# Kernel optimization log

Measured on AMD Instinct MI355X. Metric: run time of the kernel, lower is better.

## Reference

```python
import jax, jax.numpy as jnp
import numpy as np

B, T, D_IN, H = 128, 256, 512, 1024

def setup_inputs() -> dict:
    key = jax.random.key(0)
    ks = jax.random.split(key, 12)
    s = 1.0 / np.sqrt(H)
    return {
        "input": jax.random.normal(ks[0], (B, T, D_IN), jnp.float32),
        "h0": jax.random.normal(ks[1], (B, H), jnp.float32),
        "c0": jax.random.normal(ks[2], (B, H), jnp.float32),
        "ctx": jax.random.normal(ks[3], (B, T, H), jnp.float32),
        "srcmask": jax.random.randint(ks[4], (B, T), 0, 2).astype(bool),
        "W_ih": jax.random.uniform(ks[5], (4 * H, D_IN), jnp.float32, -s, s),
        "W_hh": jax.random.uniform(ks[6], (4 * H, H), jnp.float32, -s, s),
        "b_ih": jax.random.uniform(ks[7], (4 * H,), jnp.float32, -s, s),
        "b_hh": jax.random.uniform(ks[8], (4 * H,), jnp.float32, -s, s),
        "W_attn": jax.random.uniform(ks[9], (H, H), jnp.float32, -s, s),
        "W_out": jax.random.uniform(ks[10], (H, 2 * H), jnp.float32, -s, s),
    }


def reference(input, h0, c0, ctx, srcmask, W_ih, W_hh, b_ih, b_hh, W_attn, W_out):
    def step(carry, x_t):
        h, c = carry
        # LSTMCell: gate order i, f, g, o (PyTorch convention)
        gates = x_t @ W_ih.T + b_ih + h @ W_hh.T + b_hh  # [B, 4H]
        i_g, f_g, g_g, o_g = jnp.split(gates, 4, axis=-1)
        cy = jax.nn.sigmoid(f_g) * c + jax.nn.sigmoid(i_g) * jnp.tanh(g_g)
        hy = jax.nn.sigmoid(o_g) * jnp.tanh(cy)
        # Bilinear attention: score(K_j, q) = K_j^T (W_attn q)
        q = hy @ W_attn.T                                   # [B, H]
        scores = jnp.einsum("blh,bh->bl", ctx, q)          # [B, L]
        scores = jnp.where(srcmask, -jnp.inf, scores)
        probs = jax.nn.softmax(scores, axis=-1)
        wctx = jnp.einsum("bl,blh->bh", probs, ctx)        # [B, H]
        h_tilde = jnp.tanh(jnp.concatenate([wctx, hy], axis=-1) @ W_out.T)
        return (h_tilde, cy), h_tilde

    xs = jnp.transpose(input, (1, 0, 2))  # [T, B, D_IN]
    (h_f, c_f), outs = jax.lax.scan(step, (h0, c0), xs)
    output = jnp.transpose(outs, (1, 0, 2))  # [B, T, H]
    return (output, h_f, c_f)
```

## Files before the change

### kernel.cpp

```cpp
#include <hip/hip_runtime.h>
#include <hip/hip_bf16.h>
#include <math.h>

#define B_  128
#define T_  256
#define DIN 512
#define H_  1024

typedef __attribute__((ext_vector_type(8))) short bf16x8;
typedef __attribute__((ext_vector_type(4))) float f32x4;

#define GLD_LDS16(gsrc, ldst) \
  __builtin_amdgcn_global_load_lds((const __attribute__((address_space(1))) void*)(gsrc), \
                                   (__attribute__((address_space(3))) void*)(ldst), 16, 0, 0)

__device__ __forceinline__ void split_bf16(float v, __hip_bfloat16* hi, __hip_bfloat16* lo) {
    __hip_bfloat16 h = __float2bfloat16(v);
    *hi = h;
    *lo = __float2bfloat16(v - __bfloat162float(h));
}

template<int N> __device__ __forceinline__ void waitvm() {
    if constexpr (N == 0)       asm volatile("s_waitcnt vmcnt(0)" ::: "memory");
    else if constexpr (N == 10) asm volatile("s_waitcnt vmcnt(10)" ::: "memory");
    else static_assert(N == 0 || N == 10, "add vmcnt literal");
}

__global__ void bias_sum_k(const float* __restrict__ a, const float* __restrict__ b,
                           float* __restrict__ o, int n) {
    int i = blockIdx.x * blockDim.x + threadIdx.x;
    if (i < n) o[i] = a[i] + b[i];
}

__global__ void detect_mask_k(const int* __restrict__ m, int nwords, int* __restrict__ flag) {
    __shared__ int bad;
    if (threadIdx.x == 0) bad = 0;
    __syncthreads();
    for (int i = threadIdx.x; i < nwords; i += blockDim.x) {
        unsigned v = (unsigned)m[i];
        if (v > 1u) bad = 1;
    }
    __syncthreads();
    if (threadIdx.x == 0) flag[0] = bad ? 0 : 1;
}

__global__ void cvt_split_k(const float* __restrict__ s, __hip_bfloat16* __restrict__ hi,
                            __hip_bfloat16* __restrict__ lo, int n) {
    int i = blockIdx.x * 256 + threadIdx.x;
    if (i < n) split_bf16(s[i], hi + i, lo + i);
}

__global__ void wg_split_k(const float* __restrict__ Wih, const float* __restrict__ Whh,
                           __hip_bfloat16* __restrict__ Wh, __hip_bfloat16* __restrict__ Wl) {
    int i = blockIdx.x * 256 + threadIdx.x;
    int n = i / 1536, c = i - n * 1536;
    float v = (c < DIN) ? Wih[n * DIN + c] : Whh[n * H_ + (c - DIN)];
    split_bf16(v, Wh + i, Wl + i);
}

__device__ __forceinline__ void cvtx_body(int i, const float* __restrict__ xsrc,
                                          __hip_bfloat16* __restrict__ xh,
                                          __hip_bfloat16* __restrict__ xl) {
    int b = i >> 9, c = i & 511;
    split_bf16(xsrc[(size_t)b * (T_ * DIN) + c], xh + i, xl + i);
}

__global__ void cvtx_k(const float* __restrict__ xsrc, __hip_bfloat16* __restrict__ xh,
                       __hip_bfloat16* __restrict__ xl) {
    cvtx_body(blockIdx.x * 256 + threadIdx.x, xsrc, xh, xl);
}

template<int NT>
__global__ __launch_bounds__(256)
void mfma_gemm_k(const __hip_bfloat16* __restrict__ A1h, const __hip_bfloat16* __restrict__ A1l,
                 long lda1, int K1,
                 const __hip_bfloat16* __restrict__ A2h, const __hip_bfloat16* __restrict__ A2l,
                 long lda2,
                 const __hip_bfloat16* __restrict__ Wh, const __hip_bfloat16* __restrict__ Wl,
                 long ldw,
                 float* __restrict__ Cpart, long ldc, long pstride)
{
    constexpr int APL = 128 * 64 * 2;
    constexpr int BPL = 32 * 64 * 2;
    constexpr int BUFB = 2 * APL + 2 * BPL;
    __shared__ __attribute__((aligned(16))) char lds[3 * BUFB];

    const int tid = threadIdx.x;
    const int l = tid & 63, w = tid >> 6;
    const int n0 = blockIdx.x * 32;
    const int kbase = blockIdx.y * (NT * 64);
    const int wm = (w >> 1) * 64, wn = (w & 1) * 16;

    auto stage = [&](int buf, int kt) {
        char* base = lds + buf * BUFB;
        const int kb = kbase + kt * 64;
        #pragma unroll
        for (int p = 0; p < 2; ++p) {
            const __hip_bfloat16* A1 = p ? A1l : A1h;
            const __hip_bfloat16* A2 = p ? A2l : A2h;
            #pragma unroll
            for (int j = 0; j < 4; ++j) {
                int c = j * 256 + tid;
                int row = c >> 3, slot = c & 7;
                int e = kb + ((slot ^ (row & 7)) << 3);
                const __hip_bfloat16* src = (e < K1) ? (A1 + (long)row * lda1 + e)
                                                     : (A2 + (long)row * lda2 + (e - K1));
                GLD_LDS16(src, base + p * APL + ((j * 256 + (tid & 192)) << 4));
            }
            {
                int row = tid >> 3, slot = tid & 7;
                int e = kb + ((slot ^ (row & 7)) << 3);
                const __hip_bfloat16* src = (p ? Wl : Wh) + (long)(n0 + row) * ldw + e;
                GLD_LDS16(src, base + 2 * APL + p * BPL + ((tid & 192) << 4));
            }
        }
    };

    f32x4 acc[4] = {};

    stage(0, 0);
    if (NT > 1) stage(1, 1);

    for (int kt = 0; kt < NT; ++kt) {
        if (kt + 1 < NT) waitvm<10>(); else waitvm<0>();
        __builtin_amdgcn_s_barrier();
        __builtin_amdgcn_sched_barrier(0);
        if (kt + 2 < NT) stage((kt + 2) % 3, kt + 2);

        const char* base = lds + (kt % 3) * BUFB;
        #pragma unroll
        for (int ks = 0; ks < 2; ++ks) {
            bf16x8 afh[4], afl[4], bh, bl;
            #pragma unroll
            for (int mi = 0; mi < 4; ++mi) {
                int row = wm + mi * 16 + (l & 15);
                int slot = (l >> 4) + ks * 4;
                int off = row * 128 + ((slot ^ (row & 7)) << 4);
                afh[mi] = *(const bf16x8*)(base + off);
                afl[mi] = *(const bf16x8*)(base + APL + off);
            }
            {
                int row = wn + (l & 15);
                int slot = (l >> 4) + ks * 4;
                int off = row * 128 + ((slot ^ (row & 7)) << 4);
                bh = *(const bf16x8*)(base + 2 * APL + off);
                bl = *(const bf16x8*)(base + 2 * APL + BPL + off);
            }
            #pragma unroll
            for (int mi = 0; mi < 4; ++mi) {
                acc[mi] = __builtin_amdgcn_mfma_f32_16x16x32_bf16(afh[mi], bh, acc[mi], 0, 0, 0);
                acc[mi] = __builtin_amdgcn_mfma_f32_16x16x32_bf16(afl[mi], bh, acc[mi], 0, 0, 0);
                acc[mi] = __builtin_amdgcn_mfma_f32_16x16x32_bf16(afh[mi], bl, acc[mi], 0, 0, 0);
            }
        }
    }

    float* Cb = Cpart + (long)blockIdx.y * pstride;
    const int n = n0 + wn + (l & 15);
    #pragma unroll
    for (int mi = 0; mi < 4; ++mi) {
        int mbase = wm + mi * 16 + (l >> 4) * 4;
        #pragma unroll
        for (int r = 0; r < 4; ++r)
            Cb[(long)(mbase + r) * ldc + n] = acc[mi][r];
    }
}

__device__ __forceinline__ float sigmoidf_(float x) { return 1.f / (1.f + expf(-x)); }

__global__ __launch_bounds__(256)
void cell_cvtx_k(const float* __restrict__ gpart,
                 const float* __restrict__ bsum,
                 const float* __restrict__ cprev, float* __restrict__ cy,
                 __hip_bfloat16* __restrict__ AoBh, __hip_bfloat16* __restrict__ AoBl,
                 float* __restrict__ cf,
                 const float* __restrict__ xnext,
                 __hip_bfloat16* __restrict__ xh, __hip_bfloat16* __restrict__ xl)
{
    int bid = blockIdx.x;
    if (bid < 512) {
        int idx = bid * 256 + threadIdx.x;
        int b = idx >> 10, j = idx & 1023;
        const float* g0 = gpart + ((size_t)b << 12);
        const float* g1 = g0 + (size_t)128 * 4096;
        float ig = sigmoidf_(g0[j]        + g1[j]        + bsum[j]);
        float fg = sigmoidf_(g0[1024 + j] + g1[1024 + j] + bsum[1024 + j]);
        float gg = tanhf    (g0[2048 + j] + g1[2048 + j] + bsum[2048 + j]);
        float og = sigmoidf_(g0[3072 + j] + g1[3072 + j] + bsum[3072 + j]);
        float c = fg * cprev[idx] + ig * gg;
        float h = og * tanhf(c);
        cy[idx] = c;
        split_bf16(h, AoBh + (size_t)b * 2048 + 1024 + j, AoBl + (size_t)b * 2048 + 1024 + j);
        if (cf) cf[idx] = c;
    } else if (xnext) {
        cvtx_body((bid - 512) * 256 + threadIdx.x, xnext, xh, xl);
    }
}

__global__ __launch_bounds__(256)
void attn_k(const float* __restrict__ ctx, const float* __restrict__ qpart,
            const void* __restrict__ maskp, const int* __restrict__ mflag,
            __hip_bfloat16* __restrict__ AoBh, __hip_bfloat16* __restrict__ AoBl)
{
    constexpr int L = T_, H = H_;
    int b = blockIdx.x;
    const float* cb = ctx + (size_t)b * L * H;
    int tid = threadIdx.x, l = tid & 63, w = tid >> 6;
    int mode = mflag[0];

    float rq[16];
    #pragma unroll
    for (int j = 0; j < 16; ++j) {
        size_t o = (size_t)b * H + l + j * 64;
        rq[j] = qpart[o] + qpart[o + 131072] + qpart[o + 262144] + qpart[o + 393216];
    }

    float m = -INFINITY, s = 0.f, acc[16] = {};
    for (int li = w; li < L; li += 4) {
        bool msk = mode ? (((const int*)maskp)[b * L + li] != 0)
                        : (((const unsigned char*)maskp)[b * L + li] != 0);
        if (msk) continue;
        const float* cr = cb + (size_t)li * H;
        float rc[16], d = 0.f;
        #pragma unroll
        for (int j = 0; j < 16; ++j) { rc[j] = cr[l + j * 64]; d += rc[j] * rq[j]; }
        #pragma unroll
        for (int off = 1; off < 64; off <<= 1) d += __shfl_xor(d, off);
        float mn = fmaxf(m, d);
        float f = expf(m - mn);
        float p = expf(d - mn);
        s = s * f + p;
        #pragma unroll
        for (int j = 0; j < 16; ++j) acc[j] = acc[j] * f + p * rc[j];
        m = mn;
    }

    __shared__ float sacc[4][H_];
    __shared__ float sms[4][2];
    #pragma unroll
    for (int j = 0; j < 16; ++j) sacc[w][l + j * 64] = acc[j];
    if (l == 0) { sms[w][0] = m; sms[w][1] = s; }
    __syncthreads();

    float M = fmaxf(fmaxf(sms[0][0], sms[1][0]), fmaxf(sms[2][0], sms[3][0]));
    float fw[4], S = 0.f;
    #pragma unroll
    for (int ww = 0; ww < 4; ++ww) { fw[ww] = expf(sms[ww][0] - M); S += fw[ww] * sms[ww][1]; }
    float inv = 1.f / S;
    for (int k = tid; k < H; k += 256) {
        float a = sacc[0][k] * fw[0] + sacc[1][k] * fw[1] + sacc[2][k] * fw[2] + sacc[3][k] * fw[3];
        split_bf16(a * inv, AoBh + (size_t)b * 2048 + k, AoBl + (size_t)b * 2048 + k);
    }
}

__global__ __launch_bounds__(256)
void outred_k(const float* __restrict__ opart,
              __hip_bfloat16* __restrict__ hth, __hip_bfloat16* __restrict__ htl,
              float* __restrict__ outp,
              float* __restrict__ hf)
{
    int idx = blockIdx.x * 256 + threadIdx.x;
    int b = idx >> 10, j = idx & 1023;
    float v = opart[idx] + opart[idx + 131072] + opart[idx + 262144] + opart[idx + 393216];
    v = tanhf(v);
    split_bf16(v, hth + idx, htl + idx);
    outp[(size_t)b * (T_ * H_) + j] = v;
    if (hf) hf[idx] = v;
}

extern "C" void kernel_launch(void* const* d_in, const int* in_sizes, int n_in,
                              void* d_out, int out_size, void* d_ws, size_t ws_size,
                              hipStream_t stream)
{
    const float* input  = (const float*)d_in[0];
    const float* h0     = (const float*)d_in[1];
    const float* c0     = (const float*)d_in[2];
    const float* ctx    = (const float*)d_in[3];
    const void*  srcmask= d_in[4];
    const float* W_ih   = (const float*)d_in[5];
    const float* W_hh   = (const float*)d_in[6];
    const float* b_ih   = (const float*)d_in[7];
    const float* b_hh   = (const float*)d_in[8];
    const float* W_attn = (const float*)d_in[9];
    const float* W_out  = (const float*)d_in[10];

    constexpr int B = B_, T = T_, D = DIN, H = H_;

    float* f = (float*)d_ws;
    float* bsum  = f; f += 4 * H;
    float* cbuf  = f; f += (size_t)B * H;
    float* gpart = f; f += (size_t)2 * B * 4 * H;
    float* qpart = f; f += (size_t)4 * B * H;
    float* opart = f; f += (size_t)4 * B * H;
    int*   mflag = (int*)f; f += 64;
    __hip_bfloat16* p = (__hip_bfloat16*)f;
    __hip_bfloat16* Wgh = p; p += (size_t)4 * H * (D + H);
    __hip_bfloat16* Wgl = p; p += (size_t)4 * H * (D + H);
    __hip_bfloat16* Wah = p; p += (size_t)H * H;
    __hip_bfloat16* Wal = p; p += (size_t)H * H;
    __hip_bfloat16* Woh = p; p += (size_t)H * 2 * H;
    __hip_bfloat16* Wol = p; p += (size_t)H * 2 * H;
    __hip_bfloat16* hth = p; p += (size_t)B * H;
    __hip_bfloat16* htl = p; p += (size_t)B * H;
    __hip_bfloat16* AoBh = p; p += (size_t)B * 2 * H;
    __hip_bfloat16* AoBl = p; p += (size_t)B * 2 * H;
    __hip_bfloat16* xth[2], *xtl[2];
    xth[0] = p; p += (size_t)B * D;
    xtl[0] = p; p += (size_t)B * D;
    xth[1] = p; p += (size_t)B * D;
    xtl[1] = p; p += (size_t)B * D;

    float* out = (float*)d_out;
    float* hf  = out + (size_t)B * T * H;
    float* cf  = hf + (size_t)B * H;

    hipMemcpyAsync(cbuf, c0, (size_t)B * H * sizeof(float), hipMemcpyDeviceToDevice, stream);
    bias_sum_k<<<dim3(16), dim3(256), 0, stream>>>(b_ih, b_hh, bsum, 4 * H);
    detect_mask_k<<<dim3(1), dim3(256), 0, stream>>>((const int*)srcmask, B * T / 4, mflag);
    wg_split_k<<<dim3(4 * H * (D + H) / 256), dim3(256), 0, stream>>>(W_ih, W_hh, Wgh, Wgl);
    cvt_split_k<<<dim3(H * H / 256), dim3(256), 0, stream>>>(W_attn, Wah, Wal, H * H);
    cvt_split_k<<<dim3(H * 2 * H / 256), dim3(256), 0, stream>>>(W_out, Woh, Wol, H * 2 * H);
    cvt_split_k<<<dim3(B * H / 256), dim3(256), 0, stream>>>(h0, hth, htl, B * H);
    cvtx_k<<<dim3(B * D / 256), dim3(256), 0, stream>>>(input, xth[0], xtl[0]);

    dim3 blk(256);
    for (int t = 0; t < T; ++t) {
        int sl = t & 1, sn = sl ^ 1;

        mfma_gemm_k<12><<<dim3(128, 2), blk, 0, stream>>>(
            xth[sl], xtl[sl], D, D,
            hth, htl, H,
            Wgh, Wgl, D + H,
            gpart, 4 * H, (long)B * 4 * H);

        cell_cvtx_k<<<dim3(768), blk, 0, stream>>>(
            gpart, bsum, cbuf, cbuf, AoBh, AoBl, (t == T - 1) ? cf : nullptr,
            (t + 1 < T) ? input + (size_t)(t + 1) * D : nullptr, xth[sn], xtl[sn]);

        mfma_gemm_k<4><<<dim3(32, 4), blk, 0, stream>>>(
            AoBh + H, AoBl + H, 2 * H, 2 * H,
            AoBh + H, AoBl + H, 2 * H,
            Wah, Wal, H,
            qpart, H, (long)B * H);

        attn_k<<<dim3(B), blk, 0, stream>>>(ctx, qpart, srcmask, mflag, AoBh, AoBl);

        mfma_gemm_k<8><<<dim3(32, 4), blk, 0, stream>>>(
            AoBh, AoBl, 2 * H, 2 * H,
            AoBh, AoBl, 2 * H,
            Woh, Wol, 2 * H,
            opart, H, (long)B * H);

        outred_k<<<dim3(512), blk, 0, stream>>>(
            opart, hth, htl, out + (size_t)t * H, (t == T - 1) ? hf : nullptr);
    }
}
```

Baseline: 18.29 ms.

## Fuse LSTM cell into gate GEMM epilogue and output tanh into out GEMM

After: 21.53 ms. 17.7% more time.

```diff
diff --git a/kernel.cpp b/kernel.cpp
--- a/kernel.cpp
+++ b/kernel.cpp
@@ -14,22 +14,22 @@
   __builtin_amdgcn_global_load_lds((const __attribute__((address_space(1))) void*)(gsrc), \
                                    (__attribute__((address_space(3))) void*)(ldst), 16, 0, 0)
 
+#define WAITVM_(n) asm volatile("s_waitcnt vmcnt(" #n ")" ::: "memory")
+#define WAITVM(n) WAITVM_(n)
+
 __device__ __forceinline__ void split_bf16(float v, __hip_bfloat16* hi, __hip_bfloat16* lo) {
     __hip_bfloat16 h = __float2bfloat16(v);
     *hi = h;
     *lo = __float2bfloat16(v - __bfloat162float(h));
 }
 
-template<int N> __device__ __forceinline__ void waitvm() {
-    if constexpr (N == 0)       asm volatile("s_waitcnt vmcnt(0)" ::: "memory");
-    else if constexpr (N == 10) asm volatile("s_waitcnt vmcnt(10)" ::: "memory");
-    else static_assert(N == 0 || N == 10, "add vmcnt literal");
-}
-
-__global__ void bias_sum_k(const float* __restrict__ a, const float* __restrict__ b,
-                           float* __restrict__ o, int n) {
-    int i = blockIdx.x * blockDim.x + threadIdx.x;
-    if (i < n) o[i] = a[i] + b[i];
+__device__ __forceinline__ float sigmoidf_(float x) { return 1.f / (1.f + expf(-x)); }
+
+__global__ void bsum_perm_k(const float* __restrict__ bi, const float* __restrict__ bh,
+                            float* __restrict__ o) {
+    int c = blockIdx.x * 256 + threadIdx.x;
+    int srow = ((c & 3) << 10) | (c >> 2);
+    o[c] = bi[srow] + bh[srow];
 }
 
 __global__ void detect_mask_k(const int* __restrict__ m, int nwords, int* __restrict__ flag) {
@@ -50,150 +50,174 @@
     if (i < n) split_bf16(s[i], hi + i, lo + i);
 }
 
-__global__ void wg_split_k(const float* __restrict__ Wih, const float* __restrict__ Whh,
-                           __hip_bfloat16* __restrict__ Wh, __hip_bfloat16* __restrict__ Wl) {
-    int i = blockIdx.x * 256 + threadIdx.x;
-    int n = i / 1536, c = i - n * 1536;
-    float v = (c < DIN) ? Wih[n * DIN + c] : Whh[n * H_ + (c - DIN)];
+__global__ void wgp_split_k(const float* __restrict__ Wih, const float* __restrict__ Whh,
+                            __hip_bfloat16* __restrict__ Wh, __hip_bfloat16* __restrict__ Wl) {
+    long i = (long)blockIdx.x * 256 + threadIdx.x;
+    int c = (int)(i / 1536), k = (int)(i - (long)c * 1536);
+    int srow = ((c & 3) << 10) | (c >> 2);
+    float v = (k < DIN) ? Wih[(long)srow * DIN + k] : Whh[(long)srow * H_ + (k - DIN)];
     split_bf16(v, Wh + i, Wl + i);
-}
-
-__device__ __forceinline__ void cvtx_body(int i, const float* __restrict__ xsrc,
-                                          __hip_bfloat16* __restrict__ xh,
-                                          __hip_bfloat16* __restrict__ xl) {
-    int b = i >> 9, c = i & 511;
-    split_bf16(xsrc[(size_t)b * (T_ * DIN) + c], xh + i, xl + i);
 }
 
 __global__ void cvtx_k(const float* __restrict__ xsrc, __hip_bfloat16* __restrict__ xh,
                        __hip_bfloat16* __restrict__ xl) {
-    cvtx_body(blockIdx.x * 256 + threadIdx.x, xsrc, xh, xl);
-}
-
-template<int NT>
+    int i = blockIdx.x * 256 + threadIdx.x;
+    int b = i >> 9, c = i & 511;
+    split_bf16(xsrc[(long)b * (T_ * DIN) + c], xh + i, xl + i);
+}
+
+constexpr int APL = 128 * 64 * 2;
+constexpr int BPL = 32 * 64 * 2;
+constexpr int BUFB = 2 * APL + 2 * BPL;
+constexpr int LDSZ = 3 * BUFB;
+
+#define GEMM_CORE(NT, NW2, BNV, VMID, NB, KSP, A1H, A1L, LDA1, K1V, A2H, A2L, LDA2, WHP, WLP, LDW) \
+    const int n0_ = (NB) * (BNV); \
+    const int kbase_ = (KSP) * ((NT) * 64); \
+    const int wm_ = (NW2) ? (w >> 1) * 64 : w * 32; \
+    const int wn_ = (NW2) ? (w & 1) * 16 : 0; \
+    auto stage = [&](int buf, int kt) { \
+        char* base = lds + buf * BUFB; \
+        const int kb = kbase_ + kt * 64; \
+        _Pragma("unroll") \
+        for (int pp = 0; pp < 2; ++pp) { \
+            const __hip_bfloat16* A1 = pp ? (A1L) : (A1H); \
+            const __hip_bfloat16* A2 = pp ? (A2L) : (A2H); \
+            _Pragma("unroll") \
+            for (int j = 0; j < 4; ++j) { \
+                int c = j * 256 + tid; \
+                int row = c >> 3, sl2 = c & 7; \
+                int e = kb + ((sl2 ^ (row & 7)) << 3); \
+                const __hip_bfloat16* src = (e < (K1V)) ? (A1 + (long)row * (LDA1) + e) \
+                                                        : (A2 + (long)row * (LDA2) + (e - (K1V))); \
+                GLD_LDS16(src, base + pp * APL + ((j * 256 + (tid & 192)) << 4)); \
+            } \
+            if (tid < (BNV) * 8) { \
+                int row = tid >> 3, sl2 = tid & 7; \
+                int e = kb + ((sl2 ^ (row & 7)) << 3); \
+                const __hip_bfloat16* src = (pp ? (WLP) : (WHP)) + (long)(n0_ + row) * (LDW) + e; \
+                GLD_LDS16(src, base + 2 * APL + pp * BPL + ((tid & 192) << 4)); \
+            } \
+        } \
+    }; \
+    f32x4 acc[4] = {}; \
+    stage(0, 0); \
+    if ((NT) > 1) stage(1, 1); \
+    for (int kt = 0; kt < (NT); ++kt) { \
+        if (kt + 1 < (NT)) { WAITVM(VMID); } else { WAITVM(0); } \
+        __builtin_amdgcn_s_barrier(); \
+        __builtin_amdgcn_sched_barrier(0); \
+        if (kt + 2 < (NT)) stage((kt + 2) % 3, kt + 2); \
+        const char* base = lds + (kt % 3) * BUFB; \
+        _Pragma("unroll") \
+        for (int ks = 0; ks < 2; ++ks) { \
+            bf16x8 afh[4], afl[4], bh, bl; \
+            _Pragma("unroll") \
+            for (int mi = 0; mi < ((NW2) ? 4 : 2); ++mi) { \
+                int row = wm_ + mi * 16 + (l & 15); \
+                int sl2 = (l >> 4) + ks * 4; \
+                int off = row * 128 + ((sl2 ^ (row & 7)) << 4); \
+                afh[mi] = *(const bf16x8*)(base + off); \
+                afl[mi] = *(const bf16x8*)(base + APL + off); \
+            } \
+            { \
+                int row = wn_ + (l & 15); \
+                int sl2 = (l >> 4) + ks * 4; \
+                int off = row * 128 + ((sl2 ^ (row & 7)) << 4); \
+                bh = *(const bf16x8*)(base + 2 * APL + off); \
+                bl = *(const bf16x8*)(base + 2 * APL + BPL + off); \
+            } \
+            _Pragma("unroll") \
+            for (int mi = 0; mi < ((NW2) ? 4 : 2); ++mi) { \
+                acc[mi] = __builtin_amdgcn_mfma_f32_16x16x32_bf16(afh[mi], bh, acc[mi], 0, 0, 0); \
+                acc[mi] = __builtin_amdgcn_mfma_f32_16x16x32_bf16(afl[mi], bh, acc[mi], 0, 0, 0); \
+                acc[mi] = __builtin_amdgcn_mfma_f32_16x16x32_bf16(afh[mi], bl, acc[mi], 0, 0, 0); \
+            } \
+        } \
+    }
+
 __global__ __launch_bounds__(256)
-void mfma_gemm_k(const __hip_bfloat16* __restrict__ A1h, const __hip_bfloat16* __restrict__ A1l,
-                 long lda1, int K1,
-                 const __hip_bfloat16* __restrict__ A2h, const __hip_bfloat16* __restrict__ A2l,
-                 long lda2,
-                 const __hip_bfloat16* __restrict__ Wh, const __hip_bfloat16* __restrict__ Wl,
-                 long ldw,
-                 float* __restrict__ Cpart, long ldc, long pstride)
-{
-    constexpr int APL = 128 * 64 * 2;
-    constexpr int BPL = 32 * 64 * 2;
-    constexpr int BUFB = 2 * APL + 2 * BPL;
-    __shared__ __attribute__((aligned(16))) char lds[3 * BUFB];
-
+void gemm_g_k(const __hip_bfloat16* __restrict__ xh, const __hip_bfloat16* __restrict__ xl,
+              const __hip_bfloat16* __restrict__ hh, const __hip_bfloat16* __restrict__ hl,
+              const __hip_bfloat16* __restrict__ Wgh, const __hip_bfloat16* __restrict__ Wgl,
+              const float* __restrict__ bsump, float* __restrict__ cbuf,
+              __hip_bfloat16* __restrict__ AoBh, __hip_bfloat16* __restrict__ AoBl,
+              float* __restrict__ cf,
+              const float* __restrict__ input, int t,
+              __hip_bfloat16* __restrict__ nxh, __hip_bfloat16* __restrict__ nxl)
+{
+    __shared__ __attribute__((aligned(16))) char lds[LDSZ];
+    const int blk = blockIdx.x, tid = threadIdx.x;
+    const int l = tid & 63, w = tid >> 6;
+
+    GEMM_CORE(24, 1, 32, 10, blk, 0,
+              xh, xl, DIN, DIN, hh, hl, H_, Wgh, Wgl, (DIN + H_));
+
+    __syncthreads();
+    float* sg = (float*)lds;
+    {
+        float bv = bsump[n0_ + wn_ + (l & 15)];
+        #pragma unroll
+        for (int mi = 0; mi < 4; ++mi) {
+            int rbase = wm_ + mi * 16 + (l >> 4) * 4;
+            int col = wn_ + (l & 15);
+            #pragma unroll
+            for (int r = 0; r < 4; ++r)
+                sg[(rbase + r) * 36 + col] = acc[mi][r] + bv;
+        }
+    }
+    __syncthreads();
+
+    #pragma unroll
+    for (int k = 0; k < 4; ++k) {
+        int ci = k * 256 + tid;
+        int b = ci >> 3, jp = ci & 7;
+        float4 g4 = *(const float4*)&sg[b * 36 + jp * 4];
+        int j = blk * 8 + jp;
+        long idx = (long)b * H_ + j;
+        float ig = sigmoidf_(g4.x);
+        float fg = sigmoidf_(g4.y);
+        float gg = tanhf(g4.z);
+        float og = sigmoidf_(g4.w);
+        float c = fg * cbuf[idx] + ig * gg;
+        float h = og * tanhf(c);
+        cbuf[idx] = c;
+        split_bf16(h, AoBh + (long)b * 2048 + 1024 + j, AoBl + (long)b * 2048 + 1024 + j);
+        if (cf) cf[idx] = c;
+    }
+
+    if (t + 1 < T_) {
+        #pragma unroll
+        for (int k = 0; k < 2; ++k) {
+            int i2 = blk * 512 + k * 256 + tid;
+            int b2 = i2 >> 9, col = i2 & 511;
+            float v = input[((long)b2 * T_ + (t + 1)) * DIN + col];
+            split_bf16(v, nxh + i2, nxl + i2);
+        }
+    }
+}
+
+__global__ __launch_bounds__(256)
+void gemm_q_k(const __hip_bfloat16* __restrict__ AoBh, const __hip_bfloat16* __restrict__ AoBl,
+              const __hip_bfloat16* __restrict__ Wah, const __hip_bfloat16* __restrict__ Wal,
+              float* __restrict__ qpart)
+{
+    __shared__ __attribute__((aligned(16))) char lds[LDSZ];
     const int tid = threadIdx.x;
     const int l = tid & 63, w = tid >> 6;
-    const int n0 = blockIdx.x * 32;
-    const int kbase = blockIdx.y * (NT * 64);
-    const int wm = (w >> 1) * 64, wn = (w & 1) * 16;
-
-    auto stage = [&](int buf, int kt) {
-        char* base = lds + buf * BUFB;
-        const int kb = kbase + kt * 64;
-        #pragma unroll
-        for (int p = 0; p < 2; ++p) {
-            const __hip_bfloat16* A1 = p ? A1l : A1h;
-            const __hip_bfloat16* A2 = p ? A2l : A2h;
-            #pragma unroll
-            for (int j = 0; j < 4; ++j) {
-                int c = j * 256 + tid;
-                int row = c >> 3, slot = c & 7;
-                int e = kb + ((slot ^ (row & 7)) << 3);
-                const __hip_bfloat16* src = (e < K1) ? (A1 + (long)row * lda1 + e)
-                                                     : (A2 + (long)row * lda2 + (e - K1));
-                GLD_LDS16(src, base + p * APL + ((j * 256 + (tid & 192)) << 4));
-            }
-            {
-                int row = tid >> 3, slot = tid & 7;
-                int e = kb + ((slot ^ (row & 7)) << 3);
-                const __hip_bfloat16* src = (p ? Wl : Wh) + (long)(n0 + row) * ldw + e;
-                GLD_LDS16(src, base + 2 * APL + p * BPL + ((tid & 192) << 4));
-            }
-        }
-    };
-
-    f32x4 acc[4] = {};
-
-    stage(0, 0);
-    if (NT > 1) stage(1, 1);
-
-    for (int kt = 0; kt < NT; ++kt) {
-        if (kt + 1 < NT) waitvm<10>(); else waitvm<0>();
-        __builtin_amdgcn_s_barrier();
-        __builtin_amdgcn_sched_barrier(0);
-        if (kt + 2 < NT) stage((kt + 2) % 3, kt + 2);
-
-        const char* base = lds + (kt % 3) * BUFB;
-        #pragma unroll
-        for (int ks = 0; ks < 2; ++ks) {
-            bf16x8 afh[4], afl[4], bh, bl;
-            #pragma unroll
-            for (int mi = 0; mi < 4; ++mi) {
-                int row = wm + mi * 16 + (l & 15);
-                int slot = (l >> 4) + ks * 4;
-                int off = row * 128 + ((slot ^ (row & 7)) << 4);
-                afh[mi] = *(const bf16x8*)(base + off);
-                afl[mi] = *(const bf16x8*)(base + APL + off);
-            }
-            {
-                int row = wn + (l & 15);
-                int slot = (l >> 4) + ks * 4;
-                int off = row * 128 + ((slot ^ (row & 7)) << 4);
-                bh = *(const bf16x8*)(base + 2 * APL + off);
-                bl = *(const bf16x8*)(base + 2 * APL + BPL + off);
-            }
-            #pragma unroll
-            for (int mi = 0; mi < 4; ++mi) {
-                acc[mi] = __builtin_amdgcn_mfma_f32_16x16x32_bf16(afh[mi], bh, acc[mi], 0, 0, 0);
-                acc[mi] = __builtin_amdgcn_mfma_f32_16x16x32_bf16(afl[mi], bh, acc[mi], 0, 0, 0);
-                acc[mi] = __builtin_amdgcn_mfma_f32_16x16x32_bf16(afh[mi], bl, acc[mi], 0, 0, 0);
-            }
-        }
-    }
-
-    float* Cb = Cpart + (long)blockIdx.y * pstride;
-    const int n = n0 + wn + (l & 15);
+
+    GEMM_CORE(4, 1, 32, 10, (int)blockIdx.x, (int)blockIdx.y,
+              (AoBh + H_), (AoBl + H_), (2 * H_), H_,
+              (AoBh + H_), (AoBl + H_), (2 * H_), Wah, Wal, H_);
+
+    float* Cb = qpart + (long)blockIdx.y * (B_ * H_);
+    const int n = n0_ + wn_ + (l & 15);
     #pragma unroll
     for (int mi = 0; mi < 4; ++mi) {
-        int mbase = wm + mi * 16 + (l >> 4) * 4;
+        int mbase = wm_ + mi * 16 + (l >> 4) * 4;
         #pragma unroll
         for (int r = 0; r < 4; ++r)
-            Cb[(long)(mbase + r) * ldc + n] = acc[mi][r];
-    }
-}
-
-__device__ __forceinline__ float sigmoidf_(float x) { return 1.f / (1.f + expf(-x)); }
-
-__global__ __launch_bounds__(256)
-void cell_cvtx_k(const float* __restrict__ gpart,
-                 const float* __restrict__ bsum,
-                 const float* __restrict__ cprev, float* __restrict__ cy,
-                 __hip_bfloat16* __restrict__ AoBh, __hip_bfloat16* __restrict__ AoBl,
-                 float* __restrict__ cf,
-                 const float* __restrict__ xnext,
-                 __hip_bfloat16* __restrict__ xh, __hip_bfloat16* __restrict__ xl)
-{
-    int bid = blockIdx.x;
-    if (bid < 512) {
-        int idx = bid * 256 + threadIdx.x;
-        int b = idx >> 10, j = idx & 1023;
-        const float* g0 = gpart + ((size_t)b << 12);
-        const float* g1 = g0 + (size_t)128 * 4096;
-        float ig = sigmoidf_(g0[j]        + g1[j]        + bsum[j]);
-        float fg = sigmoidf_(g0[1024 + j] + g1[1024 + j] + bsum[1024 + j]);
-        float gg = tanhf    (g0[2048 + j] + g1[2048 + j] + bsum[2048 + j]);
-        float og = sigmoidf_(g0[3072 + j] + g1[3072 + j] + bsum[3072 + j]);
-        float c = fg * cprev[idx] + ig * gg;
-        float h = og * tanhf(c);
-        cy[idx] = c;
-        split_bf16(h, AoBh + (size_t)b * 2048 + 1024 + j, AoBl + (size_t)b * 2048 + 1024 + j);
-        if (cf) cf[idx] = c;
-    } else if (xnext) {
-        cvtx_body((bid - 512) * 256 + threadIdx.x, xnext, xh, xl);
+            Cb[(long)(mbase + r) * H_ + n] = acc[mi][r];
     }
 }
 
@@ -203,15 +227,17 @@
             __hip_bfloat16* __restrict__ AoBh, __hip_bfloat16* __restrict__ AoBl)
 {
     constexpr int L = T_, H = H_;
+    __shared__ float sacc[4][H_];
+    __shared__ float sms[4][2];
     int b = blockIdx.x;
-    const float* cb = ctx + (size_t)b * L * H;
+    const float* cb = ctx + (long)b * L * H;
     int tid = threadIdx.x, l = tid & 63, w = tid >> 6;
     int mode = mflag[0];
 
     float rq[16];
     #pragma unroll
     for (int j = 0; j < 16; ++j) {
-        size_t o = (size_t)b * H + l + j * 64;
+        long o = (long)b * H + l + j * 64;
         rq[j] = qpart[o] + qpart[o + 131072] + qpart[o + 262144] + qpart[o + 393216];
     }
 
@@ -220,7 +246,7 @@
         bool msk = mode ? (((const int*)maskp)[b * L + li] != 0)
                         : (((const unsigned char*)maskp)[b * L + li] != 0);
         if (msk) continue;
-        const float* cr = cb + (size_t)li * H;
+        const float* cr = cb + (long)li * H;
         float rc[16], d = 0.f;
         #pragma unroll
         for (int j = 0; j < 16; ++j) { rc[j] = cr[l + j * 64]; d += rc[j] * rq[j]; }
@@ -235,8 +261,6 @@
         m = mn;
     }
 
-    __shared__ float sacc[4][H_];
-    __shared__ float sms[4][2];
     #pragma unroll
     for (int j = 0; j < 16; ++j) sacc[w][l + j * 64] = acc[j];
     if (l == 0) { sms[w][0] = m; sms[w][1] = s; }
@@ -245,27 +269,44 @@
     float M = fmaxf(fmaxf(sms[0][0], sms[1][0]), fmaxf(sms[2][0], sms[3][0]));
     float fw[4], S = 0.f;
     #pragma unroll
-    for (int ww = 0; ww < 4; ++ww) { fw[ww] = expf(sms[ww][0] - M); S += fw[ww] * sms[ww][1]; }
+    for (int ww = 0; ww < 4; ++ww) {
+        fw[ww] = (sms[ww][0] == -INFINITY) ? 0.f : expf(sms[ww][0] - M);
+        S += fw[ww] * sms[ww][1];
+    }
     float inv = 1.f / S;
     for (int k = tid; k < H; k += 256) {
         float a = sacc[0][k] * fw[0] + sacc[1][k] * fw[1] + sacc[2][k] * fw[2] + sacc[3][k] * fw[3];
-        split_bf16(a * inv, AoBh + (size_t)b * 2048 + k, AoBl + (size_t)b * 2048 + k);
+        split_bf16(a * inv, AoBh + (long)b * 2048 + k, AoBl + (long)b * 2048 + k);
     }
 }
 
 __global__ __launch_bounds__(256)
-void outred_k(const float* __restrict__ opart,
+void gemm_o_k(const __hip_bfloat16* __restrict__ AoBh, const __hip_bfloat16* __restrict__ AoBl,
+              const __hip_bfloat16* __restrict__ Woh, const __hip_bfloat16* __restrict__ Wol,
               __hip_bfloat16* __restrict__ hth, __hip_bfloat16* __restrict__ htl,
-              float* __restrict__ outp,
-              float* __restrict__ hf)
-{
-    int idx = blockIdx.x * 256 + threadIdx.x;
-    int b = idx >> 10, j = idx & 1023;
-    float v = opart[idx] + opart[idx + 131072] + opart[idx + 262144] + opart[idx + 393216];
-    v = tanhf(v);
-    split_bf16(v, hth + idx, htl + idx);
-    outp[(size_t)b * (T_ * H_) + j] = v;
-    if (hf) hf[idx] = v;
+              float* __restrict__ out, int t, float* __restrict__ hf)
+{
+    __shared__ __attribute__((aligned(16))) char lds[LDSZ];
+    const int tid = threadIdx.x;
+    const int l = tid & 63, w = tid >> 6;
+
+    GEMM_CORE(32, 0, 16, 8, (int)blockIdx.x, 0,
+              AoBh, AoBl, (2 * H_), (2 * H_),
+              AoBh, AoBl, (2 * H_), Woh, Wol, (2 * H_));
+
+    const int j = n0_ + (l & 15);
+    #pragma unroll
+    for (int mi = 0; mi < 2; ++mi) {
+        int bbase = wm_ + mi * 16 + (l >> 4) * 4;
+        #pragma unroll
+        for (int r = 0; r < 4; ++r) {
+            int b = bbase + r;
+            float v = tanhf(acc[mi][r]);
+            split_bf16(v, hth + (long)b * H_ + j, htl + (long)b * H_ + j);
+            out[(long)b * (T_ * H_) + (long)t * H_ + j] = v;
+            if (hf) hf[(long)b * H_ + j] = v;
+        }
+    }
 }
 
 extern "C" void kernel_launch(void* const* d_in, const int* in_sizes, int n_in,
@@ -287,11 +328,9 @@
     constexpr int B = B_, T = T_, D = DIN, H = H_;
 
     float* f = (float*)d_ws;
-    float* bsum  = f; f += 4 * H;
+    float* bsump = f; f += 4 * H;
     float* cbuf  = f; f += (size_t)B * H;
-    float* gpart = f; f += (size_t)2 * B * 4 * H;
     float* qpart = f; f += (size_t)4 * B * H;
-    float* opart = f; f += (size_t)4 * B * H;
     int*   mflag = (int*)f; f += 64;
     __hip_bfloat16* p = (__hip_bfloat16*)f;
     __hip_bfloat16* Wgh = p; p += (size_t)4 * H * (D + H);
@@ -315,9 +354,9 @@
     float* cf  = hf + (size_t)B * H;
 
     hipMemcpyAsync(cbuf, c0, (size_t)B * H * sizeof(float), hipMemcpyDeviceToDevice, stream);
-    bias_sum_k<<<dim3(16), dim3(256), 0, stream>>>(b_ih, b_hh, bsum, 4 * H);
+    bsum_perm_k<<<dim3(16), dim3(256), 0, stream>>>(b_ih, b_hh, bsump);
     detect_mask_k<<<dim3(1), dim3(256), 0, stream>>>((const int*)srcmask, B * T / 4, mflag);
-    wg_split_k<<<dim3(4 * H * (D + H) / 256), dim3(256), 0, stream>>>(W_ih, W_hh, Wgh, Wgl);
+    wgp_split_k<<<dim3(4 * H * (D + H) / 256), dim3(256), 0, stream>>>(W_ih, W_hh, Wgh, Wgl);
     cvt_split_k<<<dim3(H * H / 256), dim3(256), 0, stream>>>(W_attn, Wah, Wal, H * H);
     cvt_split_k<<<dim3(H * 2 * H / 256), dim3(256), 0, stream>>>(W_out, Woh, Wol, H * 2 * H);
     cvt_split_k<<<dim3(B * H / 256), dim3(256), 0, stream>>>(h0, hth, htl, B * H);
@@ -327,31 +366,16 @@
     for (int t = 0; t < T; ++t) {
         int sl = t & 1, sn = sl ^ 1;
 
-        mfma_gemm_k<12><<<dim3(128, 2), blk, 0, stream>>>(
-            xth[sl], xtl[sl], D, D,
-            hth, htl, H,
-            Wgh, Wgl, D + H,
-            gpart, 4 * H, (long)B * 4 * H);
-
-        cell_cvtx_k<<<dim3(768), blk, 0, stream>>>(
-            gpart, bsum, cbuf, cbuf, AoBh, AoBl, (t == T - 1) ? cf : nullptr,
-            (t + 1 < T) ? input + (size_t)(t + 1) * D : nullptr, xth[sn], xtl[sn]);
-
-        mfma_gemm_k<4><<<dim3(32, 4), blk, 0, stream>>>(
-            AoBh + H, AoBl + H, 2 * H, 2 * H,
-            AoBh + H, AoBl + H, 2 * H,
-            Wah, Wal, H,
-            qpart, H, (long)B * H);
+        gemm_g_k<<<dim3(128), blk, 0, stream>>>(
+            xth[sl], xtl[sl], hth, htl, Wgh, Wgl, bsump, cbuf,
+            AoBh, AoBl, (t == T - 1) ? cf : nullptr,
+            input, t, xth[sn], xtl[sn]);
+
+        gemm_q_k<<<dim3(32, 4), blk, 0, stream>>>(AoBh, AoBl, Wah, Wal, qpart);
 
         attn_k<<<dim3(B), blk, 0, stream>>>(ctx, qpart, srcmask, mflag, AoBh, AoBl);
 
-        mfma_gemm_k<8><<<dim3(32, 4), blk, 0, stream>>>(
-            AoBh, AoBl, 2 * H, 2 * H,
-            AoBh, AoBl, 2 * H,
-            Woh, Wol, 2 * H,
-            opart, H, (long)B * H);
-
-        outred_k<<<dim3(512), blk, 0, stream>>>(
-            opart, hth, htl, out + (size_t)t * H, (t == T - 1) ? hf : nullptr);
-    }
-}
+        gemm_o_k<<<dim3(64), blk, 0, stream>>>(
+            AoBh, AoBl, Woh, Wol, hth, htl, out, t, (t == T - 1) ? hf : nullptr);
+    }
+}
```
